# Kernel tuning notes

Hardware: AMD Instinct MI355X
Metric: run time of the kernel (lower is better)

## Reference

```python
import jax, jax.numpy as jnp
import numpy as np

N_SUBGROUPS = 10
SUBSPACE = 10     # latent dims per subgroup
MAT_DIM = 8       # subgroup_size = 64 = 8*8


def setup_inputs() -> dict:
    key = jax.random.key(0)
    k1, k2 = jax.random.split(key)
    z = jax.random.normal(k1, (65536, N_SUBGROUPS * SUBSPACE), dtype=jnp.float32)
    # concatenated Lie-algebra basis: [lat_dim, mat_dim, mat_dim]
    lie_alg_basis = jax.random.normal(k2, (N_SUBGROUPS * SUBSPACE, MAT_DIM, MAT_DIM), dtype=jnp.float32) * 0.1
    return {"z": z, "lie_alg_basis": lie_alg_basis}


def reference(z, lie_alg_basis):
    # For each subgroup: lie_alg = sum_k z[:,k] * B_k  -> matrix_exp(lie_alg)
    # (train_exp with a single latent cut is mathematically identical to val_exp)
    expm_batched = jax.vmap(jax.scipy.linalg.expm)
    outs = []
    b = 0
    for i in range(N_SUBGROUPS):
        zk = z[:, b:b + SUBSPACE]                    # [B, SUBSPACE]
        Bk = lie_alg_basis[b:b + SUBSPACE]           # [SUBSPACE, m, m]
        lie_alg = jnp.einsum('bk,kij->bij', zk, Bk)  # [B, m, m]
        outs.append(expm_batched(lie_alg))           # [B, m, m]
        b += SUBSPACE
    # torch.cat(..., dim=1): [B, N_SUBGROUPS*m, m]
    return jnp.concatenate(outs, axis=1)
```

## Files before the change

### kernel.cpp

```cpp
#include <hip/hip_runtime.h>

typedef float f32x2 __attribute__((ext_vector_type(2)));
typedef float f32x4 __attribute__((ext_vector_type(4)));
typedef float f32x16 __attribute__((ext_vector_type(16)));

#define N_SUB 10
#define SUBSP 10
#define SC 0.125f

#define SLOAD16(dst, base, imm) \
  asm volatile("s_load_dwordx16 %0, %1, %2" \
               : "=s"(dst) : "s"(base), "i"(imm))
#define SWAIT4(a, b, c, d) \
  asm volatile("s_waitcnt lgkmcnt(0)" \
               : "+s"(a), "+s"(b), "+s"(c), "+s"(d))

#define SPAIR(V, j) __builtin_shufflevector(V, V, 2*(j), 2*(j)+1)

#define PKB_FMA_L(d, zp, sp) \
  asm("v_pk_fma_f32 %0, %1, %2, %0 op_sel:[0,0,0] op_sel_hi:[0,1,1]" \
      : "+v"(d) : "v"(zp), "s"(sp))
#define PKB_FMA_H(d, zp, sp) \
  asm("v_pk_fma_f32 %0, %1, %2, %0 op_sel:[1,0,0] op_sel_hi:[1,1,1]" \
      : "+v"(d) : "v"(zp), "s"(sp))
#define PKB_MUL_L(d, zp, sp) \
  asm("v_pk_mul_f32 %0, %1, %2 op_sel:[0,0] op_sel_hi:[0,1]" \
      : "=v"(d) : "v"(zp), "s"(sp))
#define PK_FMA_L(d, x, y) \
  asm("v_pk_fma_f32 %0, %1, %2, %0 op_sel:[0,0,0] op_sel_hi:[0,1,1]" \
      : "+v"(d) : "v"(x), "v"(y))
#define PK_FMA_H(d, x, y) \
  asm("v_pk_fma_f32 %0, %1, %2, %0 op_sel:[1,0,0] op_sel_hi:[1,1,1]" \
      : "+v"(d) : "v"(x), "v"(y))
#define PK_MUL_L(d, x, y) \
  asm("v_pk_mul_f32 %0, %1, %2 op_sel:[0,0] op_sel_hi:[0,1]" \
      : "=v"(d) : "v"(x), "v"(y))

#define DECLR(M, r) f32x2 M##r##0, M##r##1, M##r##2, M##r##3
#define DECLM(M) \
  DECLR(M,0); DECLR(M,1); DECLR(M,2); DECLR(M,3); \
  DECLR(M,4); DECLR(M,5); DECLR(M,6); DECLR(M,7)

#define MMCH(Z, X, Y, r, j)                  \
  PK_MUL_L(Z##r##j, X##r##0, Y##0##j);       \
  PK_FMA_H(Z##r##j, X##r##0, Y##1##j);       \
  PK_FMA_L(Z##r##j, X##r##1, Y##2##j);       \
  PK_FMA_H(Z##r##j, X##r##1, Y##3##j);       \
  PK_FMA_L(Z##r##j, X##r##2, Y##4##j);       \
  PK_FMA_H(Z##r##j, X##r##2, Y##5##j);       \
  PK_FMA_L(Z##r##j, X##r##3, Y##6##j);       \
  PK_FMA_H(Z##r##j, X##r##3, Y##7##j);
#define MMROW(Z, X, Y, r) \
  MMCH(Z,X,Y,r,0) MMCH(Z,X,Y,r,1) MMCH(Z,X,Y,r,2) MMCH(Z,X,Y,r,3)
#define MM(Z, X, Y)                                          \
  MMROW(Z,X,Y,0) MMROW(Z,X,Y,1) MMROW(Z,X,Y,2) MMROW(Z,X,Y,3) \
  MMROW(Z,X,Y,4) MMROW(Z,X,Y,5) MMROW(Z,X,Y,6) MMROW(Z,X,Y,7)

#define BLDK2(F, Kv, ra, rb)                                  \
  F(A##ra##0, zz, SPAIR(Kv,0)); F(A##ra##1, zz, SPAIR(Kv,1)); \
  F(A##ra##2, zz, SPAIR(Kv,2)); F(A##ra##3, zz, SPAIR(Kv,3)); \
  F(A##rb##0, zz, SPAIR(Kv,4)); F(A##rb##1, zz, SPAIR(Kv,5)); \
  F(A##rb##2, zz, SPAIR(Kv,6)); F(A##rb##3, zz, SPAIR(Kv,7));
#define KSTEP(koff, F)                                        \
  {                                                           \
    f32x16 K0, K1, K2, K3;                                    \
    SLOAD16(K0, bp, (koff)*256 + 0);                          \
    SLOAD16(K1, bp, (koff)*256 + 64);                         \
    SLOAD16(K2, bp, (koff)*256 + 128);                        \
    SLOAD16(K3, bp, (koff)*256 + 192);                        \
    SWAIT4(K0, K1, K2, K3);                                   \
    BLDK2(F, K0, 0, 1) BLDK2(F, K1, 2, 3)                     \
    BLDK2(F, K2, 4, 5) BLDK2(F, K3, 6, 7)                     \
  }

#define LCROW(P, X, Y, ca, cb, r)                            \
  P##r##0 = (ca)*X##r##0 + (cb)*Y##r##0;                     \
  P##r##1 = (ca)*X##r##1 + (cb)*Y##r##1;                     \
  P##r##2 = (ca)*X##r##2 + (cb)*Y##r##2;                     \
  P##r##3 = (ca)*X##r##3 + (cb)*Y##r##3;
#define LC(P, X, Y, ca, cb)                                  \
  LCROW(P,X,Y,ca,cb,0) LCROW(P,X,Y,ca,cb,1) LCROW(P,X,Y,ca,cb,2) \
  LCROW(P,X,Y,ca,cb,3) LCROW(P,X,Y,ca,cb,4) LCROW(P,X,Y,ca,cb,5) \
  LCROW(P,X,Y,ca,cb,6) LCROW(P,X,Y,ca,cb,7)
#define AXROW(P, X, Q, cc, r)                                \
  P##r##0 = (cc)*X##r##0 + Q##r##0;                          \
  P##r##1 = (cc)*X##r##1 + Q##r##1;                          \
  P##r##2 = (cc)*X##r##2 + Q##r##2;                          \
  P##r##3 = (cc)*X##r##3 + Q##r##3;
#define AXPY(P, X, Q, cc)                                    \
  AXROW(P,X,Q,cc,0) AXROW(P,X,Q,cc,1) AXROW(P,X,Q,cc,2)      \
  AXROW(P,X,Q,cc,3) AXROW(P,X,Q,cc,4) AXROW(P,X,Q,cc,5)      \
  AXROW(P,X,Q,cc,6) AXROW(P,X,Q,cc,7)

#define ADD_DIAG(M, c)                                       \
  M##00[0] += (c); M##10[1] += (c); M##21[0] += (c); M##31[1] += (c); \
  M##42[0] += (c); M##52[1] += (c); M##63[0] += (c); M##73[1] += (c);

#define STROW(M, r, outp) {                                  \
  f32x4 w0 = __builtin_shufflevector(M##r##0, M##r##1, 0,1,2,3); \
  f32x4 w1 = __builtin_shufflevector(M##r##2, M##r##3, 0,1,2,3); \
  *(f32x4*)((outp) + (r)*8)     = w0;                        \
  *(f32x4*)((outp) + (r)*8 + 4) = w1; }
#define STORE(M, outp)                                       \
  STROW(M,0,outp) STROW(M,1,outp) STROW(M,2,outp) STROW(M,3,outp) \
  STROW(M,4,outp) STROW(M,5,outp) STROW(M,6,outp) STROW(M,7,outp)

#define EXPM(M, outp) {                                      \
    DECLM(S); MM(S, M, M)                                    \
    DECLM(P); LC(P, S, M, c8, c7) ADD_DIAG(P, c6)            \
    DECLM(Q); MM(Q, S, P)                                    \
    AXPY(P, M, Q, c5) ADD_DIAG(P, c4)                        \
    MM(Q, S, P)                                              \
    AXPY(P, M, Q, c3) ADD_DIAG(P, c2)                        \
    MM(Q, S, P)                                              \
    AXPY(P, M, Q, 1.0f) ADD_DIAG(P, 1.0f)                    \
    MM(Q, P, P) MM(P, Q, Q) MM(Q, P, P)                      \
    STORE(Q, outp) }

__global__ __launch_bounds__(64)
__attribute__((amdgpu_waves_per_eu(2, 4)))
void lie_expm_kernel(const float* __restrict__ z,
                     const float* __restrict__ basis,
                     float* __restrict__ out) {
  const int lane = threadIdx.x & 63;
  const int W = blockIdx.x;
  const int g  = W % N_SUB;
  const int b  = (W / N_SUB) * 64 + lane;

  const float* bp = basis + g * (SUBSP * 64);

  const float* zrow = z + (size_t)b * (N_SUB * SUBSP) + g * SUBSP;
  const f32x2 zv0 = *(const f32x2*)(zrow + 0) * SC;
  const f32x2 zv1 = *(const f32x2*)(zrow + 2) * SC;
  const f32x2 zv2 = *(const f32x2*)(zrow + 4) * SC;
  const f32x2 zv3 = *(const f32x2*)(zrow + 6) * SC;
  const f32x2 zv4 = *(const f32x2*)(zrow + 8) * SC;

  DECLM(A);
  { const f32x2 zz = zv0; KSTEP(0, PKB_MUL_L) }
  { const f32x2 zz = zv0; KSTEP(1, PKB_FMA_H) }
  { const f32x2 zz = zv1; KSTEP(2, PKB_FMA_L) }
  { const f32x2 zz = zv1; KSTEP(3, PKB_FMA_H) }
  { const f32x2 zz = zv2; KSTEP(4, PKB_FMA_L) }
  { const f32x2 zz = zv2; KSTEP(5, PKB_FMA_H) }
  { const f32x2 zz = zv3; KSTEP(6, PKB_FMA_L) }
  { const f32x2 zz = zv3; KSTEP(7, PKB_FMA_H) }
  { const f32x2 zz = zv4; KSTEP(8, PKB_FMA_L) }
  { const f32x2 zz = zv4; KSTEP(9, PKB_FMA_H) }

  const float c2 = 0.5f, c3 = 1.0f / 6.0f, c4 = 1.0f / 24.0f,
              c5 = 1.0f / 120.0f, c6 = 1.0f / 720.0f,
              c7 = 1.0f / 5040.0f, c8 = 1.0f / 40320.0f;

  float* outp = out + ((size_t)b * N_SUB + g) * 64;
  EXPM(A, outp);
}

extern "C" void kernel_launch(void* const* d_in, const int* in_sizes, int n_in,
                              void* d_out, int out_size, void* d_ws, size_t ws_size,
                              hipStream_t stream) {
  const float* z = (const float*)d_in[0];
  const float* basis = (const float*)d_in[1];
  float* out = (float*)d_out;

  const int batch = in_sizes[0] / (N_SUB * SUBSP);
  const int grid = batch / 64 * N_SUB;

  lie_expm_kernel<<<grid, 64, 0, stream>>>(z, basis, out);
}
```

Baseline: 91.14 us.

## Process four batch chunks per wave with prefetch of next z rows

Each wave now loops over four consecutive 64-sample chunks for its subgroup instead of one, and the grid shrinks by four. The z values for the next chunk are loaded before the current chunk's matrix exponential runs, so the load latency is hidden behind compute. This amortizes launch and wave-setup cost, but it cuts the number of waves and therefore the parallelism available to fill the GPU. It also re-issues the scalar basis loads on every iteration.

```diff
diff --git a/kernel.cpp b/kernel.cpp
--- a/kernel.cpp
+++ b/kernel.cpp
@@ -6,6 +6,7 @@
 
 #define N_SUB 10
 #define SUBSP 10
+#define NITER 4
 #define SC 0.125f
 
 #define SLOAD16(dst, base, imm) \
@@ -124,36 +125,51 @@
                      float* __restrict__ out) {
   const int lane = threadIdx.x & 63;
   const int W = blockIdx.x;
-  const int g  = W % N_SUB;
-  const int b  = (W / N_SUB) * 64 + lane;
+  const int g = W % N_SUB;
+  const int cb = W / N_SUB;
 
   const float* bp = basis + g * (SUBSP * 64);
-
-  const float* zrow = z + (size_t)b * (N_SUB * SUBSP) + g * SUBSP;
-  const f32x2 zv0 = *(const f32x2*)(zrow + 0) * SC;
-  const f32x2 zv1 = *(const f32x2*)(zrow + 2) * SC;
-  const f32x2 zv2 = *(const f32x2*)(zrow + 4) * SC;
-  const f32x2 zv3 = *(const f32x2*)(zrow + 6) * SC;
-  const f32x2 zv4 = *(const f32x2*)(zrow + 8) * SC;
-
-  DECLM(A);
-  { const f32x2 zz = zv0; KSTEP(0, PKB_MUL_L) }
-  { const f32x2 zz = zv0; KSTEP(1, PKB_FMA_H) }
-  { const f32x2 zz = zv1; KSTEP(2, PKB_FMA_L) }
-  { const f32x2 zz = zv1; KSTEP(3, PKB_FMA_H) }
-  { const f32x2 zz = zv2; KSTEP(4, PKB_FMA_L) }
-  { const f32x2 zz = zv2; KSTEP(5, PKB_FMA_H) }
-  { const f32x2 zz = zv3; KSTEP(6, PKB_FMA_L) }
-  { const f32x2 zz = zv3; KSTEP(7, PKB_FMA_H) }
-  { const f32x2 zz = zv4; KSTEP(8, PKB_FMA_L) }
-  { const f32x2 zz = zv4; KSTEP(9, PKB_FMA_H) }
 
   const float c2 = 0.5f, c3 = 1.0f / 6.0f, c4 = 1.0f / 24.0f,
               c5 = 1.0f / 120.0f, c6 = 1.0f / 720.0f,
               c7 = 1.0f / 5040.0f, c8 = 1.0f / 40320.0f;
 
-  float* outp = out + ((size_t)b * N_SUB + g) * 64;
-  EXPM(A, outp);
+  int b = cb * (64 * NITER) + lane;
+  const float* zrow = z + (size_t)b * (N_SUB * SUBSP) + g * SUBSP;
+  f32x2 zv0 = *(const f32x2*)(zrow + 0);
+  f32x2 zv1 = *(const f32x2*)(zrow + 2);
+  f32x2 zv2 = *(const f32x2*)(zrow + 4);
+  f32x2 zv3 = *(const f32x2*)(zrow + 6);
+  f32x2 zv4 = *(const f32x2*)(zrow + 8);
+
+#pragma unroll 1
+  for (int it = 0; it < NITER; ++it) {
+    DECLM(A);
+    { const f32x2 zz = zv0 * SC; KSTEP(0, PKB_MUL_L) }
+    { const f32x2 zz = zv0 * SC; KSTEP(1, PKB_FMA_H) }
+    { const f32x2 zz = zv1 * SC; KSTEP(2, PKB_FMA_L) }
+    { const f32x2 zz = zv1 * SC; KSTEP(3, PKB_FMA_H) }
+    { const f32x2 zz = zv2 * SC; KSTEP(4, PKB_FMA_L) }
+    { const f32x2 zz = zv2 * SC; KSTEP(5, PKB_FMA_H) }
+    { const f32x2 zz = zv3 * SC; KSTEP(6, PKB_FMA_L) }
+    { const f32x2 zz = zv3 * SC; KSTEP(7, PKB_FMA_H) }
+    { const f32x2 zz = zv4 * SC; KSTEP(8, PKB_FMA_L) }
+    { const f32x2 zz = zv4 * SC; KSTEP(9, PKB_FMA_H) }
+
+    const int bn = b + ((it < NITER - 1) ? 64 : 0);
+    const float* zn = z + (size_t)bn * (N_SUB * SUBSP) + g * SUBSP;
+    f32x2 n0 = *(const f32x2*)(zn + 0);
+    f32x2 n1 = *(const f32x2*)(zn + 2);
+    f32x2 n2 = *(const f32x2*)(zn + 4);
+    f32x2 n3 = *(const f32x2*)(zn + 6);
+    f32x2 n4 = *(const f32x2*)(zn + 8);
+
+    float* outp = out + ((size_t)b * N_SUB + g) * 64;
+    EXPM(A, outp);
+
+    zv0 = n0; zv1 = n1; zv2 = n2; zv3 = n3; zv4 = n4;
+    b = bn;
+  }
 }
 
 extern "C" void kernel_launch(void* const* d_in, const int* in_sizes, int n_in,
@@ -164,7 +180,7 @@
   float* out = (float*)d_out;
 
   const int batch = in_sizes[0] / (N_SUB * SUBSP);
-  const int grid = batch / 64 * N_SUB;
+  const int grid = (batch / (64 * NITER)) * N_SUB;
 
   lie_expm_kernel<<<grid, 64, 0, stream>>>(z, basis, out);
 }
```

Result: slower. 105.4 us (+15.7%).
